# Optimization experiments

Measured on AMD Instinct MI355X. Metric: run time of the kernel, lower is better.

The kernel has to match this reference:

```python
import jax, jax.numpy as jnp
import numpy as np

B, A, BOARD, D = 64, 32, 64, 5
TAU_FAC, TAU_INH = 50.0, 20.0
LR_FAC, LR_INH = 0.0002, 0.0001
COLL_WINDOW = 10.0
SAFE_THRESH = 0.7
ALIGN_THRESH = 0.6


def setup_inputs() -> dict:
    key = jax.random.key(0)
    ks = jax.random.split(key, 7)
    positions = jax.random.uniform(ks[0], (B, A, 2), jnp.float32, 0.0, BOARD)
    goals = jax.random.uniform(ks[1], (B, A, 2), jnp.float32, 0.0, BOARD)
    spike_outputs = jax.random.uniform(ks[2], (B, A, D), jnp.float32)
    fac_traces = jax.random.uniform(ks[3], (B, A, BOARD, BOARD, D), jnp.float32)
    inh_traces = jax.random.uniform(ks[4], (B, A, BOARD, BOARD, D), jnp.float32)
    collision_history = jax.random.uniform(ks[5], (B, A, BOARD, BOARD), jnp.float32)
    collisions = jax.random.bernoulli(ks[6], 0.2, (B, A))
    return {"positions": positions, "goals": goals, "spike_outputs": spike_outputs,
            "fac_traces": fac_traces, "inh_traces": inh_traces,
            "collision_history": collision_history, "collisions": collisions}


def reference(positions, goals, spike_outputs, fac_traces, inh_traces,
              collision_history, collisions):
    # action deltas for the 5 movement directions
    deltas = jnp.array([[0, 0], [1, 0], [0, 1], [-1, 0], [0, -1]], jnp.float32)

    # 1) exponential STDP trace decay (bulk elementwise over 5D tensors)
    fac = fac_traces * jnp.exp(-1.0 / TAU_FAC)
    inh = inh_traces * jnp.exp(-1.0 / TAU_INH)

    # 2) collision history: decay + scatter-add at clamped integer positions
    pos_i = positions.astype(jnp.int32)                        # torch .long() truncation (positions >= 0)
    x = jnp.clip(pos_i[..., 0], 0, BOARD - 1)                  # [B, A]
    y = jnp.clip(pos_i[..., 1], 0, BOARD - 1)
    bi = jnp.arange(collision_history.shape[0])[:, None]
    ai = jnp.arange(collision_history.shape[1])[None, :]
    ch = collision_history * (1.0 - 1.0 / COLL_WINDOW)
    ch = ch.at[bi, ai, y, x].add(collisions.astype(jnp.float32) / COLL_WINDOW)

    # 3) region safety: gather collision rate at each agent's cell
    safety = 1.0 - jnp.clip(ch[bi, ai, y, x], 0.0, 1.0)        # [B, A]

    # 4) goal alignment for all directions at once
    gv = goals - positions                                     # [B, A, 2]
    gvn = gv / (jnp.linalg.norm(gv, axis=-1, keepdims=True) + 1e-8)
    align = (jnp.einsum('bav,dv->bad', gvn, deltas) + 1.0) / 2.0  # [B, A, D]

    # 5) facilitation / inhibition conditions and position-indexed scatter updates
    spike_cond = spike_outputs > 0.5
    safe = (safety > SAFE_THRESH)[..., None]
    fac_cond = spike_cond & safe & (align > ALIGN_THRESH)
    inh_cond = spike_cond & (~safe | (align <= 1.0 - ALIGN_THRESH))
    fac = fac.at[bi, ai, y, x].add(LR_FAC * fac_cond.astype(jnp.float32))
    inh = inh.at[bi, ai, y, x].add(LR_INH * inh_cond.astype(jnp.float32))

    return fac, inh, ch, safety
```

## Files before the change

kernel.cpp:

```cpp
#include <hip/hip_runtime.h>

static constexpr int B_ = 64, A_ = 32, BOARD_ = 64, D_ = 5;
static constexpr long long FACN = (long long)B_ * A_ * BOARD_ * BOARD_ * D_;
static constexpr long long CHN  = (long long)B_ * A_ * BOARD_ * BOARD_;
static constexpr int NAG = B_ * A_;

static constexpr float FAC_DECAY = 0.9801986733067553f;
static constexpr float INH_DECAY = 0.9512294245007140f;

typedef float f32x4 __attribute__((ext_vector_type(4)));

__global__ __launch_bounds__(256) void bulk_kernel(
    const f32x4* __restrict__ fac_in, const f32x4* __restrict__ inh_in,
    const f32x4* __restrict__ ch_in, f32x4* __restrict__ out)
{
    const int FACV = (int)(FACN / 4);
    const int C = 11264;
    const int t = threadIdx.x;
    const int base = blockIdx.x * C;

    auto ldgrp = [&](int G, f32x4 v[4], float& c) {
        const f32x4* __restrict__ s;
        if (G < FACV)          { s = fac_in + G;             c = FAC_DECAY; }
        else if (G < 2 * FACV) { s = inh_in + (G - FACV);    c = INH_DECAY; }
        else                   { s = ch_in + (G - 2 * FACV); c = 0.9f; }
        v[0] = __builtin_nontemporal_load(&s[t]);
        v[1] = __builtin_nontemporal_load(&s[t + 256]);
        v[2] = __builtin_nontemporal_load(&s[t + 512]);
        v[3] = __builtin_nontemporal_load(&s[t + 768]);
    };

    f32x4 v[4]; float c;
    ldgrp(base, v, c);
    int off = 0;
    while (true) {
        f32x4 w[4]; float c2;
        const int noff = off + 1024;
        if (noff < C) ldgrp(base + noff, w, c2);
        f32x4* __restrict__ d = out + base + off;
        __builtin_nontemporal_store(v[0] * c, &d[t]);
        __builtin_nontemporal_store(v[1] * c, &d[t + 256]);
        __builtin_nontemporal_store(v[2] * c, &d[t + 512]);
        __builtin_nontemporal_store(v[3] * c, &d[t + 768]);
        if (noff >= C) break;
        v[0] = w[0]; v[1] = w[1]; v[2] = w[2]; v[3] = w[3]; c = c2;
        off = noff;
    }
}

__global__ __launch_bounds__(64) void agent_kernel(
    const float* __restrict__ pos, const float* __restrict__ goal,
    const float* __restrict__ spike,
    const float* __restrict__ fac_in, const float* __restrict__ inh_in,
    const float* __restrict__ ch_in,
    const void* __restrict__ coll,
    float* __restrict__ out)
{
    __shared__ int s_w4, s_h2;
    if (threadIdx.x == 0) { s_w4 = 1; s_h2 = 1; }
    __syncthreads();
    {
        const unsigned int* cw = (const unsigned int*)coll;
        for (int k = threadIdx.x; k < 512; k += 64) {
            unsigned int w = cw[k];
            if (!(w == 0u || w == 1u || w == 0x3F800000u)) s_w4 = 0;
            unsigned int lo = w & 0xFFFFu, hi = w >> 16;
            if (!((lo == 0u || lo == 1u || lo == 0x3F80u || lo == 0x3C00u) &&
                  (hi == 0u || hi == 1u || hi == 0x3F80u || hi == 0x3C00u)))
                s_h2 = 0;
        }
    }
    __syncthreads();
    const int f = s_w4 ? 4 : (s_h2 ? 2 : 1);

    const int tid = blockIdx.x * 64 + threadIdx.x;
    const int idx = tid >> 3;
    const int d   = tid & 7;
    if (idx >= NAG || d >= 6) return;

    float px = pos[idx * 2 + 0];
    float py = pos[idx * 2 + 1];
    int x = min(BOARD_ - 1, max(0, (int)px));
    int y = min(BOARD_ - 1, max(0, (int)py));
    long long cell = ((long long)idx * BOARD_ + y) * BOARD_ + x;

    bool c;
    if (f == 4)      c = ((const unsigned int*)coll)[idx] != 0u;
    else if (f == 2) c = ((const unsigned short*)coll)[idx] != 0u;
    else             c = ((const unsigned char*)coll)[idx] != 0u;

    float chv = ch_in[cell] * 0.9f + (c ? 0.1f : 0.0f);
    float safety = 1.0f - fminf(fmaxf(chv, 0.0f), 1.0f);

    if (d == 5) {
        const long long CHOFF  = 2 * FACN;
        const long long SAFOFF = CHOFF + CHN;
        out[CHOFF + cell] = chv;
        out[SAFOFF + idx] = safety;
        return;
    }

    bool safe = safety > 0.7f;

    float gx = goal[idx * 2 + 0] - px;
    float gy = goal[idx * 2 + 1] - py;
    float n = sqrtf(gx * gx + gy * gy) + 1e-8f;
    float gnx = gx / n, gny = gy / n;
    float al = (d == 0) ? 0.5f
             : (d == 1) ? (gnx + 1.0f) * 0.5f
             : (d == 2) ? (gny + 1.0f) * 0.5f
             : (d == 3) ? (1.0f - gnx) * 0.5f
                        : (1.0f - gny) * 0.5f;

    long long cd = cell * D_ + d;
    bool sp = spike[idx * D_ + d] > 0.5f;
    bool fc = sp && safe && (al > 0.6f);
    bool ic = sp && (!safe || (al <= 0.4f));
    out[cd]        = fac_in[cd] * FAC_DECAY + (fc ? 0.0002f : 0.0f);
    out[FACN + cd] = inh_in[cd] * INH_DECAY + (ic ? 0.0001f : 0.0f);
}

extern "C" void kernel_launch(void* const* d_in, const int* in_sizes, int n_in,
                              void* d_out, int out_size, void* d_ws, size_t ws_size,
                              hipStream_t stream) {
    const float* pos   = (const float*)d_in[0];
    const float* goal  = (const float*)d_in[1];
    const float* spike = (const float*)d_in[2];
    const float* fac   = (const float*)d_in[3];
    const float* inh   = (const float*)d_in[4];
    const float* ch    = (const float*)d_in[5];
    const void*  coll  = d_in[6];
    float* out = (float*)d_out;

    hipLaunchKernelGGL(bulk_kernel, dim3(2048), dim3(256), 0, stream,
                       (const f32x4*)fac, (const f32x4*)inh, (const f32x4*)ch, (f32x4*)out);
    hipLaunchKernelGGL(agent_kernel, dim3(256), dim3(64), 0, stream,
                       pos, goal, spike, fac, inh, ch, coll, out);
}
```

Before: 144.6 us.

## Fuse agent scatter fixups into bulk decay kernel with per-block ownership

```diff
diff --git a/kernel.cpp b/kernel.cpp
--- a/kernel.cpp
+++ b/kernel.cpp
@@ -4,51 +4,17 @@
 static constexpr long long FACN = (long long)B_ * A_ * BOARD_ * BOARD_ * D_;
 static constexpr long long CHN  = (long long)B_ * A_ * BOARD_ * BOARD_;
 static constexpr int NAG = B_ * A_;
+static constexpr int SL  = BOARD_ * BOARD_ * D_;
+static constexpr int SLC = BOARD_ * BOARD_;
 
 static constexpr float FAC_DECAY = 0.9801986733067553f;
 static constexpr float INH_DECAY = 0.9512294245007140f;
 
 typedef float f32x4 __attribute__((ext_vector_type(4)));
 
-__global__ __launch_bounds__(256) void bulk_kernel(
-    const f32x4* __restrict__ fac_in, const f32x4* __restrict__ inh_in,
-    const f32x4* __restrict__ ch_in, f32x4* __restrict__ out)
-{
-    const int FACV = (int)(FACN / 4);
-    const int C = 11264;
-    const int t = threadIdx.x;
-    const int base = blockIdx.x * C;
-
-    auto ldgrp = [&](int G, f32x4 v[4], float& c) {
-        const f32x4* __restrict__ s;
-        if (G < FACV)          { s = fac_in + G;             c = FAC_DECAY; }
-        else if (G < 2 * FACV) { s = inh_in + (G - FACV);    c = INH_DECAY; }
-        else                   { s = ch_in + (G - 2 * FACV); c = 0.9f; }
-        v[0] = __builtin_nontemporal_load(&s[t]);
-        v[1] = __builtin_nontemporal_load(&s[t + 256]);
-        v[2] = __builtin_nontemporal_load(&s[t + 512]);
-        v[3] = __builtin_nontemporal_load(&s[t + 768]);
-    };
-
-    f32x4 v[4]; float c;
-    ldgrp(base, v, c);
-    int off = 0;
-    while (true) {
-        f32x4 w[4]; float c2;
-        const int noff = off + 1024;
-        if (noff < C) ldgrp(base + noff, w, c2);
-        f32x4* __restrict__ d = out + base + off;
-        __builtin_nontemporal_store(v[0] * c, &d[t]);
-        __builtin_nontemporal_store(v[1] * c, &d[t + 256]);
-        __builtin_nontemporal_store(v[2] * c, &d[t + 512]);
-        __builtin_nontemporal_store(v[3] * c, &d[t + 768]);
-        if (noff >= C) break;
-        v[0] = w[0]; v[1] = w[1]; v[2] = w[2]; v[3] = w[3]; c = c2;
-        off = noff;
-    }
-}
-
-__global__ __launch_bounds__(64) void agent_kernel(
+__global__ __launch_bounds__(256) void fused_kernel(
+    const f32x4* __restrict__ fac4, const f32x4* __restrict__ inh4,
+    const f32x4* __restrict__ ch4, f32x4* __restrict__ out4,
     const float* __restrict__ pos, const float* __restrict__ goal,
     const float* __restrict__ spike,
     const float* __restrict__ fac_in, const float* __restrict__ inh_in,
@@ -56,12 +22,49 @@
     const void* __restrict__ coll,
     float* __restrict__ out)
 {
+    const int FACV = (int)(FACN / 4);
+    const int C = 11264;
+    const int t = threadIdx.x;
+    const int bid = blockIdx.x;
+    const int base = bid * C;
+
     __shared__ int s_w4, s_h2;
-    if (threadIdx.x == 0) { s_w4 = 1; s_h2 = 1; }
+    if (t == 0) { s_w4 = 1; s_h2 = 1; }
     __syncthreads();
+
+    auto ldgrp = [&](int G, f32x4 v[4], float& c) {
+        const f32x4* __restrict__ s;
+        if (G < FACV)          { s = fac4 + G;             c = FAC_DECAY; }
+        else if (G < 2 * FACV) { s = inh4 + (G - FACV);    c = INH_DECAY; }
+        else                   { s = ch4 + (G - 2 * FACV); c = 0.9f; }
+        v[0] = __builtin_nontemporal_load(&s[t]);
+        v[1] = __builtin_nontemporal_load(&s[t + 256]);
+        v[2] = __builtin_nontemporal_load(&s[t + 512]);
+        v[3] = __builtin_nontemporal_load(&s[t + 768]);
+    };
+
+    {
+        f32x4 v[4]; float c;
+        ldgrp(base, v, c);
+        int off = 0;
+        while (true) {
+            f32x4 w[4]; float c2;
+            const int noff = off + 1024;
+            if (noff < C) ldgrp(base + noff, w, c2);
+            f32x4* __restrict__ d = out4 + base + off;
+            __builtin_nontemporal_store(v[0] * c, &d[t]);
+            __builtin_nontemporal_store(v[1] * c, &d[t + 256]);
+            __builtin_nontemporal_store(v[2] * c, &d[t + 512]);
+            __builtin_nontemporal_store(v[3] * c, &d[t + 768]);
+            if (noff >= C) break;
+            v[0] = w[0]; v[1] = w[1]; v[2] = w[2]; v[3] = w[3]; c = c2;
+            off = noff;
+        }
+    }
+
     {
         const unsigned int* cw = (const unsigned int*)coll;
-        for (int k = threadIdx.x; k < 512; k += 64) {
+        for (int k = t; k < 512; k += 256) {
             unsigned int w = cw[k];
             if (!(w == 0u || w == 1u || w == 0x3F800000u)) s_w4 = 0;
             unsigned int lo = w & 0xFFFFu, hi = w >> 16;
@@ -70,54 +73,103 @@
                 s_h2 = 0;
         }
     }
+    __threadfence_block();
     __syncthreads();
     const int f = s_w4 ? 4 : (s_h2 ? 2 : 1);
 
-    const int tid = blockIdx.x * 64 + threadIdx.x;
-    const int idx = tid >> 3;
-    const int d   = tid & 7;
-    if (idx >= NAG || d >= 6) return;
+    const long long CF = 45056;
+    const long long F0 = (long long)bid * CF, F1 = F0 + CF;
 
-    float px = pos[idx * 2 + 0];
-    float py = pos[idx * 2 + 1];
-    int x = min(BOARD_ - 1, max(0, (int)px));
-    int y = min(BOARD_ - 1, max(0, (int)py));
-    long long cell = ((long long)idx * BOARD_ + y) * BOARD_ + x;
+    auto fix_agent = [&](int ia, int region) {
+        float px = pos[ia * 2 + 0];
+        float py = pos[ia * 2 + 1];
+        int x = min(BOARD_ - 1, max(0, (int)px));
+        int y = min(BOARD_ - 1, max(0, (int)py));
+        int lcell = y * BOARD_ + x;
 
-    bool c;
-    if (f == 4)      c = ((const unsigned int*)coll)[idx] != 0u;
-    else if (f == 2) c = ((const unsigned short*)coll)[idx] != 0u;
-    else             c = ((const unsigned char*)coll)[idx] != 0u;
+        bool c;
+        if (f == 4)      c = ((const unsigned int*)coll)[ia] != 0u;
+        else if (f == 2) c = ((const unsigned short*)coll)[ia] != 0u;
+        else             c = ((const unsigned char*)coll)[ia] != 0u;
 
-    float chv = ch_in[cell] * 0.9f + (c ? 0.1f : 0.0f);
-    float safety = 1.0f - fminf(fmaxf(chv, 0.0f), 1.0f);
+        float chv = ch_in[(long long)ia * SLC + lcell] * 0.9f + (c ? 0.1f : 0.0f);
+        float safety = 1.0f - fminf(fmaxf(chv, 0.0f), 1.0f);
 
-    if (d == 5) {
-        const long long CHOFF  = 2 * FACN;
-        const long long SAFOFF = CHOFF + CHN;
-        out[CHOFF + cell] = chv;
-        out[SAFOFF + idx] = safety;
-        return;
+        if (region == 2) {
+            long long fl = 2 * FACN + (long long)ia * SLC + lcell;
+            if (fl >= F0 && fl < F1) out[fl] = chv;
+            return;
+        }
+
+        bool safe = safety > 0.7f;
+        float gx = goal[ia * 2 + 0] - px;
+        float gy = goal[ia * 2 + 1] - py;
+        float n = sqrtf(gx * gx + gy * gy) + 1e-8f;
+        float gnx = gx / n, gny = gy / n;
+        float align[5];
+        align[0] = 0.5f;
+        align[1] = (gnx + 1.0f) * 0.5f;
+        align[2] = (gny + 1.0f) * 0.5f;
+        align[3] = (1.0f - gnx) * 0.5f;
+        align[4] = (1.0f - gny) * 0.5f;
+
+        long long cdb = (long long)ia * SL + (long long)lcell * D_;
+#pragma unroll
+        for (int d = 0; d < D_; ++d) {
+            bool sp = spike[ia * D_ + d] > 0.5f;
+            long long fl;
+            float v;
+            if (region == 0) {
+                bool fc = sp && safe && (align[d] > 0.6f);
+                v = fac_in[cdb + d] * FAC_DECAY + (fc ? 0.0002f : 0.0f);
+                fl = cdb + d;
+            } else {
+                bool ic = sp && (!safe || (align[d] <= 0.4f));
+                v = inh_in[cdb + d] * INH_DECAY + (ic ? 0.0001f : 0.0f);
+                fl = FACN + cdb + d;
+            }
+            if (fl >= F0 && fl < F1) out[fl] = v;
+        }
+    };
+
+    if (t < 4) {
+        long long a1 = min(F1, FACN);
+        if (F0 < a1) {
+            int ia = (int)(F0 / SL) + t;
+            int iaMax = (int)((a1 - 1) / SL);
+            if (ia <= iaMax && ia < NAG) fix_agent(ia, 0);
+        }
     }
-
-    bool safe = safety > 0.7f;
-
-    float gx = goal[idx * 2 + 0] - px;
-    float gy = goal[idx * 2 + 1] - py;
-    float n = sqrtf(gx * gx + gy * gy) + 1e-8f;
-    float gnx = gx / n, gny = gy / n;
-    float al = (d == 0) ? 0.5f
-             : (d == 1) ? (gnx + 1.0f) * 0.5f
-             : (d == 2) ? (gny + 1.0f) * 0.5f
-             : (d == 3) ? (1.0f - gnx) * 0.5f
-                        : (1.0f - gny) * 0.5f;
-
-    long long cd = cell * D_ + d;
-    bool sp = spike[idx * D_ + d] > 0.5f;
-    bool fc = sp && safe && (al > 0.6f);
-    bool ic = sp && (!safe || (al <= 0.4f));
-    out[cd]        = fac_in[cd] * FAC_DECAY + (fc ? 0.0002f : 0.0f);
-    out[FACN + cd] = inh_in[cd] * INH_DECAY + (ic ? 0.0001f : 0.0f);
+    else if (t >= 8 && t < 12) {
+        long long b0 = max(F0, FACN), b1 = min(F1, 2 * FACN);
+        if (b0 < b1) {
+            int ia = (int)((b0 - FACN) / SL) + (t - 8);
+            int iaMax = (int)((b1 - FACN - 1) / SL);
+            if (ia <= iaMax && ia < NAG) fix_agent(ia, 1);
+        }
+    }
+    else if (t >= 16 && t < 32) {
+        long long c0 = max(F0, 2 * FACN), c1 = min(F1, 2 * FACN + CHN);
+        if (c0 < c1) {
+            int ia = (int)((c0 - 2 * FACN) / SLC) + (t - 16);
+            int iaMax = (int)((c1 - 2 * FACN - 1) / SLC);
+            if (ia <= iaMax && ia < NAG) fix_agent(ia, 2);
+        }
+    }
+    else if (t == 40) {
+        int ia = bid;
+        float px = pos[ia * 2 + 0];
+        float py = pos[ia * 2 + 1];
+        int x = min(BOARD_ - 1, max(0, (int)px));
+        int y = min(BOARD_ - 1, max(0, (int)py));
+        int lcell = y * BOARD_ + x;
+        bool c;
+        if (f == 4)      c = ((const unsigned int*)coll)[ia] != 0u;
+        else if (f == 2) c = ((const unsigned short*)coll)[ia] != 0u;
+        else             c = ((const unsigned char*)coll)[ia] != 0u;
+        float chv = ch_in[(long long)ia * SLC + lcell] * 0.9f + (c ? 0.1f : 0.0f);
+        out[2 * FACN + CHN + ia] = 1.0f - fminf(fmaxf(chv, 0.0f), 1.0f);
+    }
 }
 
 extern "C" void kernel_launch(void* const* d_in, const int* in_sizes, int n_in,
@@ -132,8 +184,7 @@
     const void*  coll  = d_in[6];
     float* out = (float*)d_out;
 
-    hipLaunchKernelGGL(bulk_kernel, dim3(2048), dim3(256), 0, stream,
-                       (const f32x4*)fac, (const f32x4*)inh, (const f32x4*)ch, (f32x4*)out);
-    hipLaunchKernelGGL(agent_kernel, dim3(256), dim3(64), 0, stream,
+    hipLaunchKernelGGL(fused_kernel, dim3(2048), dim3(256), 0, stream,
+                       (const f32x4*)fac, (const f32x4*)inh, (const f32x4*)ch, (f32x4*)out,
                        pos, goal, spike, fac, inh, ch, coll, out);
 }
```

Result: no change. 142.5 us (-1.4%).
